# Kernel tuning notes

Hardware: AMD Instinct MI355X
Metric: run time of the kernel (lower is better)

Reference implementation:

```python
import jax, jax.numpy as jnp
import numpy as np

N_HEAD = 16
N_KV = 4
HEAD_DIM = 128
ROPE_BASE = 10000.0
YARN_ORIG = 2048
YARN_TARGET = 8192
YARN_ALPHA = 1.0
YARN_BETA = 1.0
SOFTCAP = 50.0


def _yarn_freqs(seq_len, start=0):
    # inv_freq with YaRN scaling: stretch by (target/orig)**alpha, magnitude 1/beta
    inv_freq = 1.0 / (ROPE_BASE ** (jnp.arange(0, HEAD_DIM, 2, dtype=jnp.float32) / HEAD_DIM))
    scale = (YARN_TARGET / YARN_ORIG) ** YARN_ALPHA
    inv_freq = inv_freq / scale * (1.0 / max(YARN_BETA, 1e-6))
    pos = jnp.arange(start, start + seq_len, dtype=jnp.float32)
    return pos[:, None] * inv_freq[None, :]  # [T, D/2]


def _apply_rope(x, freqs):
    # x: [B, H, T, D], interleaved even/odd rotation
    x_even = x[..., ::2]
    x_odd = x[..., 1::2]
    cos = jnp.cos(freqs)[None, None]  # [1,1,T,D/2]
    sin = jnp.sin(freqs)[None, None]
    y_even = x_even * cos - x_odd * sin
    y_odd = x_odd * cos + x_even * sin
    y = jnp.stack([y_even, y_odd], axis=-1).reshape(x.shape)
    return y


def setup_inputs() -> dict:
    key = jax.random.key(0)
    k1, k2, k3 = jax.random.split(key, 3)
    B, T, C = 2, 2048, 2048
    qkv_dim = (N_HEAD + 2 * N_KV) * HEAD_DIM  # 3072
    x = jax.random.normal(k1, (B, T, C), dtype=jnp.float32)
    w_qkv = jax.random.normal(k2, (C, qkv_dim), dtype=jnp.float32) * (1.0 / np.sqrt(C))
    w_o = jax.random.normal(k3, (C, C), dtype=jnp.float32) * (1.0 / np.sqrt(C))
    return {"x": x, "w_qkv": w_qkv, "w_o": w_o}


def reference(x, w_qkv, w_o):
    B, T, C = x.shape
    qkv = x @ w_qkv  # [B, T, (H+2*Hkv)*D]
    q_dim = N_HEAD * HEAD_DIM
    kv_dim = N_KV * HEAD_DIM
    q = qkv[..., :q_dim].reshape(B, T, N_HEAD, HEAD_DIM).transpose(0, 2, 1, 3)
    k = qkv[..., q_dim:q_dim + kv_dim].reshape(B, T, N_KV, HEAD_DIM).transpose(0, 2, 1, 3)
    v = qkv[..., q_dim + kv_dim:].reshape(B, T, N_KV, HEAD_DIM).transpose(0, 2, 1, 3)

    freqs = _yarn_freqs(T)
    q = _apply_rope(q, freqs)
    k = _apply_rope(k, freqs)

    # GQA: expand kv heads to query heads
    rep = N_HEAD // N_KV
    k = jnp.repeat(k, rep, axis=1)
    v = jnp.repeat(v, rep, axis=1)

    scores = jnp.einsum('bhqd,bhkd->bhqk', q, k) / jnp.sqrt(jnp.float32(HEAD_DIM))
    scores = SOFTCAP * jnp.tanh(scores / SOFTCAP)
    causal = jnp.tril(jnp.ones((T, T), dtype=bool))
    scores = jnp.where(causal[None, None], scores, jnp.float32(-1e9))
    attn = jax.nn.softmax(scores.astype(jnp.float32), axis=-1).astype(q.dtype)
    out = jnp.einsum('bhqk,bhkd->bhqd', attn, v)
    out = out.transpose(0, 2, 1, 3).reshape(B, T, C)
    return out @ w_o
```

## Files before the change

kernel.cpp:

```cpp
#include <hip/hip_runtime.h>
#include <hip/hip_bf16.h>

typedef __attribute__((ext_vector_type(8))) __bf16 bf16x8;
typedef __attribute__((ext_vector_type(2))) __bf16 bf16x2;
typedef __attribute__((ext_vector_type(4))) float f32x4;

#define T_SEQ 2048
#define C_DIM 2048
#define QKV_DIM 3072
#define NKV 4
#define HD 128

#define AS1 __attribute__((address_space(1)))
#define AS3 __attribute__((address_space(3)))

__device__ __forceinline__ unsigned short f2bf(float x) {
    __hip_bfloat16 h = __float2bfloat16(x);
    return __builtin_bit_cast(unsigned short, h);
}
__device__ __forceinline__ float bf2f(unsigned short u) {
    unsigned int i = ((unsigned int)u) << 16;
    return __builtin_bit_cast(float, i);
}
__device__ __forceinline__ unsigned int pkbf(float lo, float hi) {
#if __has_builtin(__builtin_amdgcn_cvt_pk_bf16_f32)
    bf16x2 r = __builtin_amdgcn_cvt_pk_bf16_f32(lo, hi);
    return __builtin_bit_cast(unsigned int, r);
#else
    return ((unsigned int)f2bf(hi) << 16) | (unsigned int)f2bf(lo);
#endif
}
__device__ __forceinline__ f32x4 mfma16(bf16x8 a, bf16x8 b, f32x4 c) {
    return __builtin_amdgcn_mfma_f32_16x16x32_bf16(a, b, c, 0, 0, 0);
}
__device__ __forceinline__ void gload_lds16(const void* g, void* l) {
    __builtin_amdgcn_global_load_lds((const AS1 unsigned int*)g,
                                     (AS3 unsigned int*)l, 16, 0, 0);
}

__global__ __launch_bounds__(256) void cast_f32_to_bf16(
        const float* __restrict__ in, unsigned short* __restrict__ out, int n4) {
    int i = blockIdx.x * 256 + threadIdx.x;
    if (i >= n4) return;
    float4 v = ((const float4*)in)[i];
    uint2 o;
    o.x = pkbf(v.x, v.y);
    o.y = pkbf(v.z, v.w);
    ((uint2*)out)[i] = o;
}

__global__ __launch_bounds__(256) void transpose_cast_f32_bf16(
        const float* __restrict__ in, unsigned short* __restrict__ out,
        int rows, int cols) {
    __shared__ float tile[32][33];
    int c0 = blockIdx.x * 32, r0 = blockIdx.y * 32;
    int tx = threadIdx.x, ty = threadIdx.y;
    #pragma unroll
    for (int i = 0; i < 4; i++)
        tile[ty + 8 * i][tx] = in[(size_t)(r0 + ty + 8 * i) * cols + c0 + tx];
    __syncthreads();
    #pragma unroll
    for (int i = 0; i < 4; i++)
        out[(size_t)(c0 + ty + 8 * i) * rows + r0 + tx] = f2bf(tile[tx][ty + 8 * i]);
}

__global__ __launch_bounds__(256) void pack_k(
        const unsigned short* __restrict__ qkv, unsigned short* __restrict__ kpack) {
    int sid = blockIdx.x;
    int tid = threadIdx.x;
    int row = tid >> 4;
    int chunk = tid & 15;
    int b = sid >> 9, kv = (sid >> 7) & 3, st = sid & 127;
    int t_ = st * 16 + row;
    const unsigned short* src =
        qkv + (size_t)(b * T_SEQ + t_) * QKV_DIM + 2048 + kv * HD + chunk * 8;
    unsigned short* dst = kpack + (size_t)sid * 2048 + chunk * 128 + row * 8;
    *(uint4*)dst = *(const uint4*)src;
}

__global__ __launch_bounds__(256) void pack_v(
        const unsigned short* __restrict__ qkv, unsigned short* __restrict__ vpack) {
    __shared__ unsigned short tile[32][33];
    int c0 = blockIdx.x * 32;
    int r0 = blockIdx.y * 32;
    int tx = threadIdx.x, ty = threadIdx.y;
    #pragma unroll
    for (int i = 0; i < 4; i++)
        tile[ty + 8 * i][tx] =
            qkv[(size_t)(r0 + ty + 8 * i) * QKV_DIM + 2560 + c0 + tx];
    __syncthreads();
    #pragma unroll
    for (int i = 0; i < 4; i++) {
        int dcol = c0 + ty + 8 * i;
        int kv = dcol >> 7, d = dcol & 127;
        int r = r0 + tx;
        int b = r >> 11, t = r & (T_SEQ - 1);
        vpack[(size_t)((b * NKV + kv) * 64 + (t >> 5)) * 4096 +
              (d >> 4) * 512 + ((t >> 3) & 3) * 128 + (d & 15) * 8 + (t & 7)] =
            tile[tx][ty + 8 * i];
    }
}

__global__ __launch_bounds__(256) void yarn_tab_kernel(float2* __restrict__ tab) {
    int idx = blockIdx.x * 256 + threadIdx.x;
    int t = idx >> 6, i = idx & 63;
    float inv = 0.25f * exp2f(-(float)i * (13.287712379549449f / 64.0f));
    float ang = (float)t * inv;
    float s, c;
    __sincosf(ang, &s, &c);
    tab[idx] = make_float2(c, s);
}

__global__ __launch_bounds__(256) void rope_kernel(
        unsigned short* __restrict__ qkv, const float2* __restrict__ tab) {
    int row = blockIdx.x;
    int t = row & (T_SEQ - 1);
    const float2* tb = tab + t * 64;
    for (int p = threadIdx.x; p < 1280; p += 256) {
        int head = p >> 6, i = p & 63;
        float2 cs = tb[i];
        size_t idx = (size_t)row * QKV_DIM + head * 128 + 2 * i;
        unsigned int u = *(const unsigned int*)(qkv + idx);
        float e = bf2f((unsigned short)(u & 0xffff));
        float o = bf2f((unsigned short)(u >> 16));
        *(unsigned int*)(qkv + idx) = pkbf(e * cs.x - o * cs.y, o * cs.x + e * cs.y);
    }
}

template <int OUT_BF16>
__global__ __launch_bounds__(256) void gemm_bt(
        const unsigned short* __restrict__ A, const unsigned short* __restrict__ Bt,
        void* __restrict__ Cout, int M, int N, int K) {
    __shared__ __align__(16) unsigned short As[128 * 32];
    __shared__ __align__(16) unsigned short Bs[128 * 32];
    int tid = threadIdx.x;
    int m0 = blockIdx.y * 128, n0 = blockIdx.x * 128;
    int wave = tid >> 6, lane = tid & 63;
    int wm = (wave & 1) * 64, wn = (wave >> 1) * 64;
    int l15 = lane & 15, quad = lane >> 4;
    int lrow = lane >> 2, lcol = (lane & 3) * 8;

    f32x4 zf = {0.f, 0.f, 0.f, 0.f};
    f32x4 acc[4][4];
    #pragma unroll
    for (int i = 0; i < 4; i++)
        #pragma unroll
        for (int j = 0; j < 4; j++) acc[i][j] = zf;

    int ca = wave * 2;
    const unsigned short* gA = A + (size_t)(m0 + ca * 16 + lrow) * K + lcol;
    const unsigned short* gB = Bt + (size_t)(n0 + ca * 16 + lrow) * K + lcol;

    for (int k0 = 0; k0 < K; k0 += 32) {
        gload_lds16(gA + k0, &As[ca * 512]);
        gload_lds16(gA + k0 + 16 * (size_t)K, &As[ca * 512 + 512]);
        gload_lds16(gB + k0, &Bs[ca * 512]);
        gload_lds16(gB + k0 + 16 * (size_t)K, &Bs[ca * 512 + 512]);
        __syncthreads();
        bf16x8 af[4], bfr[4];
        #pragma unroll
        for (int i = 0; i < 4; i++)
            af[i] = *(const bf16x8*)&As[(wm + i * 16 + l15) * 32 + quad * 8];
        #pragma unroll
        for (int i = 0; i < 4; i++)
            bfr[i] = *(const bf16x8*)&Bs[(wn + i * 16 + l15) * 32 + quad * 8];
        #pragma unroll
        for (int mi = 0; mi < 4; mi++)
            #pragma unroll
            for (int ni = 0; ni < 4; ni++)
                acc[mi][ni] = mfma16(af[mi], bfr[ni], acc[mi][ni]);
        __syncthreads();
    }
    #pragma unroll
    for (int mi = 0; mi < 4; mi++)
        #pragma unroll
        for (int ni = 0; ni < 4; ni++) {
            int row = m0 + wm + mi * 16 + quad * 4;
            int col = n0 + wn + ni * 16 + l15;
            #pragma unroll
            for (int r = 0; r < 4; r++) {
                float v = acc[mi][ni][r];
                if (OUT_BF16)
                    ((unsigned short*)Cout)[(size_t)(row + r) * N + col] = f2bf(v);
                else
                    ((float*)Cout)[(size_t)(row + r) * N + col] = v;
            }
        }
}

__device__ __forceinline__ void attn_pair(
        const unsigned short* __restrict__ qkv,
        const unsigned short* __restrict__ kpack,
        const unsigned short* __restrict__ vpack,
        unsigned short* __restrict__ attn_out,
        unsigned int* __restrict__ pT, float* __restrict__ comb,
        int b, int h, int j, int wave, int lane) {
    int l15 = lane & 15, quad = lane >> 4;
    int kv = h >> 2;
    f32x4 zf = {0.f, 0.f, 0.f, 0.f};

    const float K1 = 0.0051006972f;
    const float K2 = -144.26950408889634f;
    const float K3 = 72.13475204444817f;

    const unsigned short* kb_ = kpack + ((size_t)(b * NKV + kv) * 128) * 2048 + lane * 8;
    const unsigned short* vb_ = vpack + ((size_t)(b * NKV + kv) * 64) * 4096 + lane * 8;

    for (int pass = 0; pass < 2; pass++) {
        int qt = pass ? (127 - j) : j;
        int n = (qt >> 1) + 1;
        int half = n >> 1;
        int lo = wave ? half : 0;
        int hi = wave ? n : half;

        const unsigned short* qp =
            qkv + (size_t)(b * T_SEQ + qt * 16 + l15) * QKV_DIM + h * HD + quad * 8;
        bf16x8 aq[4];
        #pragma unroll
        for (int c = 0; c < 4; c++) aq[c] = *(const bf16x8*)(qp + c * 32);

        f32x4 oacc[8];
        #pragma unroll
        for (int d = 0; d < 8; d++) oacc[d] = zf;
        float lsum = 0.f;
        int qglob = qt * 16 + l15;

        if (lo < hi) {
            bf16x8 KA[8], KB[8];
            auto loadK = [&](bf16x8* K, int t) {
                const unsigned short* a = kb_ + (size_t)t * 4096;
                #pragma unroll
                for (int c = 0; c < 4; c++) {
                    K[c]     = *(const bf16x8*)(a + c * 512);
                    K[4 + c] = *(const bf16x8*)(a + 2048 + c * 512);
                }
            };
            auto step = [&](const bf16x8* K, unsigned int* buf, int t,
                            bf16x8* Kpre, bool do_pre) {
                const unsigned short* v0 = vb_ + (size_t)t * 4096;
                bf16x8 Vv[8];
                #pragma unroll
                for (int dd = 0; dd < 8; dd++)
                    Vv[dd] = *(const bf16x8*)(v0 + dd * 512);
                if (do_pre) loadK(Kpre, t + 1);
                f32x4 s0 = zf, s1 = zf;
                #pragma unroll
                for (int c = 0; c < 4; c++) {
                    s0 = mfma16(K[c], aq[c], s0);
                    s1 = mfma16(K[4 + c], aq[c], s1);
                }
                bool masked = (t == n - 1);
                float p0[4], p1[4];
                int kb = t * 32 + quad * 4;
                #pragma unroll
                for (int r = 0; r < 4; r++) {
                    float e0 = exp2f(s0[r] * K1);
                    float e1 = exp2f(s1[r] * K1);
                    float q0 = exp2f(fmaf(K2, __builtin_amdgcn_rcpf(e0 + 1.f), K3));
                    float q1 = exp2f(fmaf(K2, __builtin_amdgcn_rcpf(e1 + 1.f), K3));
                    if (masked) {
                        q0 = (kb + r <= qglob) ? q0 : 0.f;
                        q1 = (kb + 16 + r <= qglob) ? q1 : 0.f;
                    }
                    p0[r] = q0; p1[r] = q1;
                    lsum += q0 + q1;
                }
                unsigned int d0 = pkbf(p0[0], p0[1]), d1 = pkbf(p0[2], p0[3]);
                unsigned int d2 = pkbf(p1[0], p1[1]), d3 = pkbf(p1[2], p1[3]);
                unsigned int* wp = buf + l15 * 20 + quad * 2;
                *(uint2*)wp = make_uint2(d0, d1);
                *(uint2*)(wp + 8) = make_uint2(d2, d3);
                __asm__ volatile("s_waitcnt lgkmcnt(0)" ::: "memory");
                bf16x8 bp = *(const bf16x8*)(buf + l15 * 20 + quad * 4);
                #pragma unroll
                for (int dd = 0; dd < 8; dd++) oacc[dd] = mfma16(Vv[dd], bp, oacc[dd]);
            };

            loadK(KA, lo);
            int t = lo;
            while (true) {
                bool last = (t == hi - 1);
                step(KA, pT, t, KB, !last);
                if (last) break;
                t++;
                last = (t == hi - 1);
                step(KB, pT + 320, t, KA, !last);
                if (last) break;
                t++;
            }
        }

        float* cl = comb + lane * 34;
        if (wave == 0) {
            #pragma unroll
            for (int dd = 0; dd < 8; dd++)
                #pragma unroll
                for (int r = 0; r < 4; r++) cl[dd * 4 + r] = oacc[dd][r];
            cl[32] = lsum;
        }
        __syncthreads();
        if (wave == 1) {
            #pragma unroll
            for (int dd = 0; dd < 8; dd++)
                #pragma unroll
                for (int r = 0; r < 4; r++) oacc[dd][r] += cl[dd * 4 + r];
            lsum += cl[32];
            float l = lsum;
            l += __shfl_xor(l, 16);
            l += __shfl_xor(l, 32);
            float rl = __builtin_amdgcn_rcpf(l);
            unsigned short* op = attn_out +
                (size_t)(b * T_SEQ + qt * 16 + l15) * C_DIM + h * HD + quad * 4;
            #pragma unroll
            for (int dd = 0; dd < 8; dd++) {
                unsigned int u0 = pkbf(oacc[dd][0] * rl, oacc[dd][1] * rl);
                unsigned int u1 = pkbf(oacc[dd][2] * rl, oacc[dd][3] * rl);
                *(uint2*)(op + dd * 16) = make_uint2(u0, u1);
            }
        }
        __syncthreads();
    }
}

__global__ __launch_bounds__(128, 2) void attn_kernel(
        const unsigned short* __restrict__ qkv,
        const unsigned short* __restrict__ kpack,
        const unsigned short* __restrict__ vpack,
        unsigned short* __restrict__ attn_out) {
    __shared__ __align__(16) unsigned int pT[2][640];
    __shared__ float comb[64 * 34];
    int bid = blockIdx.x;
    int g = bid & 7, i = bid >> 3;
    int b = g >> 2, kv = g & 3;
    int hh = (i >> 6) & 3, j = i & 63;
    int h = kv * 4 + hh;
    int wave = threadIdx.x >> 6, lane = threadIdx.x & 63;
    attn_pair(qkv, kpack, vpack, attn_out, pT[wave], comb, b, h, j, wave, lane);
}

extern "C" void kernel_launch(void* const* d_in, const int* in_sizes, int n_in,
                              void* d_out, int out_size, void* d_ws, size_t ws_size,
                              hipStream_t stream) {
    (void)in_sizes; (void)n_in; (void)out_size; (void)ws_size;
    const float* x = (const float*)d_in[0];
    const float* w_qkv = (const float*)d_in[1];
    const float* w_o = (const float*)d_in[2];
    char* ws = (char*)d_ws;

    unsigned short* xbf   = (unsigned short*)(ws);
    unsigned short* wqkvT = (unsigned short*)(ws + 16777216);
    unsigned short* woT   = (unsigned short*)(ws + 29360128);
    unsigned short* qkv   = (unsigned short*)(ws + 37748736);
    unsigned short* kpack = (unsigned short*)(ws + 16777216);
    unsigned short* vpack = (unsigned short*)(ws + 20971520);
    float2*         tab   = (float2*)(ws + 62914560);
    unsigned short* attn  = xbf;

    cast_f32_to_bf16<<<8192, 256, 0, stream>>>(x, xbf, 2097152);
    transpose_cast_f32_bf16<<<dim3(96, 64), dim3(32, 8), 0, stream>>>(w_qkv, wqkvT, 2048, 3072);
    transpose_cast_f32_bf16<<<dim3(64, 64), dim3(32, 8), 0, stream>>>(w_o, woT, 2048, 2048);
    yarn_tab_kernel<<<512, 256, 0, stream>>>(tab);
    gemm_bt<1><<<dim3(24, 32), 256, 0, stream>>>(xbf, wqkvT, qkv, 4096, 3072, 2048);
    rope_kernel<<<4096, 256, 0, stream>>>(qkv, tab);
    pack_k<<<1024, 256, 0, stream>>>(qkv, kpack);
    pack_v<<<dim3(16, 128), dim3(32, 8), 0, stream>>>(qkv, vpack);
    attn_kernel<<<2048, 128, 0, stream>>>(qkv, kpack, vpack, attn);
    gemm_bt<0><<<dim3(16, 32), 256, 0, stream>>>(attn, woT, d_out, 4096, 2048, 2048);
}
```

Before: 350.6 us.

## Process two GQA query heads per attention block to reuse K/V loads

Each attention block now handles two query heads that share a KV head, so every K and V tile loaded from global memory feeds twice as many MFMAs. The grid is halved and the shared P buffers and combine buffers are doubled. The final cross-wave reduction is split so each wave finalises one head. Register pressure roughly doubles for the accumulators, and the launch_bounds occupancy hint was dropped, which may lower occupancy or cause spills.

```diff
diff --git a/kernel.cpp b/kernel.cpp
--- a/kernel.cpp
+++ b/kernel.cpp
@@ -194,9 +194,9 @@
         const unsigned short* __restrict__ vpack,
         unsigned short* __restrict__ attn_out,
         unsigned int* __restrict__ pT, float* __restrict__ comb,
-        int b, int h, int j, int wave, int lane) {
+        int b, int hA, int j, int wave, int lane) {
     int l15 = lane & 15, quad = lane >> 4;
-    int kv = h >> 2;
+    int kv = hA >> 2;
     f32x4 zf = {0.f, 0.f, 0.f, 0.f};
 
     const float K1 = 0.0051006972f;
@@ -205,6 +205,9 @@
 
     const unsigned short* kb_ = kpack + ((size_t)(b * NKV + kv) * 128) * 2048 + lane * 8;
     const unsigned short* vb_ = vpack + ((size_t)(b * NKV + kv) * 64) * 4096 + lane * 8;
+
+    float* myStore = comb + (wave * 64 + lane) * 34;
+    float* peer    = comb + ((1 - wave) * 64 + lane) * 34;
 
     for (int pass = 0; pass < 2; pass++) {
         int qt = pass ? (127 - j) : j;
@@ -214,15 +217,18 @@
         int hi = wave ? n : half;
 
         const unsigned short* qp =
-            qkv + (size_t)(b * T_SEQ + qt * 16 + l15) * QKV_DIM + h * HD + quad * 8;
-        bf16x8 aq[4];
-        #pragma unroll
-        for (int c = 0; c < 4; c++) aq[c] = *(const bf16x8*)(qp + c * 32);
-
-        f32x4 oacc[8];
-        #pragma unroll
-        for (int d = 0; d < 8; d++) oacc[d] = zf;
-        float lsum = 0.f;
+            qkv + (size_t)(b * T_SEQ + qt * 16 + l15) * QKV_DIM + hA * HD + quad * 8;
+        bf16x8 aqA[4], aqB[4];
+        #pragma unroll
+        for (int c = 0; c < 4; c++) {
+            aqA[c] = *(const bf16x8*)(qp + c * 32);
+            aqB[c] = *(const bf16x8*)(qp + HD + c * 32);
+        }
+
+        f32x4 oA[8], oB[8];
+        #pragma unroll
+        for (int d = 0; d < 8; d++) { oA[d] = zf; oB[d] = zf; }
+        float lsA = 0.f, lsB = 0.f;
         int qglob = qt * 16 + l15;
 
         if (lo < hi) {
@@ -243,37 +249,47 @@
                 for (int dd = 0; dd < 8; dd++)
                     Vv[dd] = *(const bf16x8*)(v0 + dd * 512);
                 if (do_pre) loadK(Kpre, t + 1);
-                f32x4 s0 = zf, s1 = zf;
+                f32x4 s0A = zf, s1A = zf, s0B = zf, s1B = zf;
                 #pragma unroll
                 for (int c = 0; c < 4; c++) {
-                    s0 = mfma16(K[c], aq[c], s0);
-                    s1 = mfma16(K[4 + c], aq[c], s1);
+                    s0A = mfma16(K[c],     aqA[c], s0A);
+                    s1A = mfma16(K[4 + c], aqA[c], s1A);
+                    s0B = mfma16(K[c],     aqB[c], s0B);
+                    s1B = mfma16(K[4 + c], aqB[c], s1B);
                 }
                 bool masked = (t == n - 1);
-                float p0[4], p1[4];
+                float p0A[4], p1A[4], p0B[4], p1B[4];
                 int kb = t * 32 + quad * 4;
                 #pragma unroll
                 for (int r = 0; r < 4; r++) {
-                    float e0 = exp2f(s0[r] * K1);
-                    float e1 = exp2f(s1[r] * K1);
-                    float q0 = exp2f(fmaf(K2, __builtin_amdgcn_rcpf(e0 + 1.f), K3));
-                    float q1 = exp2f(fmaf(K2, __builtin_amdgcn_rcpf(e1 + 1.f), K3));
+                    float e0A = exp2f(s0A[r] * K1), e1A = exp2f(s1A[r] * K1);
+                    float e0B = exp2f(s0B[r] * K1), e1B = exp2f(s1B[r] * K1);
+                    float q0A = exp2f(fmaf(K2, __builtin_amdgcn_rcpf(e0A + 1.f), K3));
+                    float q1A = exp2f(fmaf(K2, __builtin_amdgcn_rcpf(e1A + 1.f), K3));
+                    float q0B = exp2f(fmaf(K2, __builtin_amdgcn_rcpf(e0B + 1.f), K3));
+                    float q1B = exp2f(fmaf(K2, __builtin_amdgcn_rcpf(e1B + 1.f), K3));
                     if (masked) {
-                        q0 = (kb + r <= qglob) ? q0 : 0.f;
-                        q1 = (kb + 16 + r <= qglob) ? q1 : 0.f;
+                        bool m0 = (kb + r <= qglob), m1 = (kb + 16 + r <= qglob);
+                        q0A = m0 ? q0A : 0.f;  q1A = m1 ? q1A : 0.f;
+                        q0B = m0 ? q0B : 0.f;  q1B = m1 ? q1B : 0.f;
                     }
-                    p0[r] = q0; p1[r] = q1;
-                    lsum += q0 + q1;
+                    p0A[r] = q0A; p1A[r] = q1A; lsA += q0A + q1A;
+                    p0B[r] = q0B; p1B[r] = q1B; lsB += q0B + q1B;
                 }
-                unsigned int d0 = pkbf(p0[0], p0[1]), d1 = pkbf(p0[2], p0[3]);
-                unsigned int d2 = pkbf(p1[0], p1[1]), d3 = pkbf(p1[2], p1[3]);
-                unsigned int* wp = buf + l15 * 20 + quad * 2;
-                *(uint2*)wp = make_uint2(d0, d1);
-                *(uint2*)(wp + 8) = make_uint2(d2, d3);
+                unsigned int* wpA = buf + l15 * 20 + quad * 2;
+                unsigned int* wpB = wpA + 320;
+                *(uint2*)wpA       = make_uint2(pkbf(p0A[0], p0A[1]), pkbf(p0A[2], p0A[3]));
+                *(uint2*)(wpA + 8) = make_uint2(pkbf(p1A[0], p1A[1]), pkbf(p1A[2], p1A[3]));
+                *(uint2*)wpB       = make_uint2(pkbf(p0B[0], p0B[1]), pkbf(p0B[2], p0B[3]));
+                *(uint2*)(wpB + 8) = make_uint2(pkbf(p1B[0], p1B[1]), pkbf(p1B[2], p1B[3]));
                 __asm__ volatile("s_waitcnt lgkmcnt(0)" ::: "memory");
-                bf16x8 bp = *(const bf16x8*)(buf + l15 * 20 + quad * 4);
-                #pragma unroll
-                for (int dd = 0; dd < 8; dd++) oacc[dd] = mfma16(Vv[dd], bp, oacc[dd]);
+                bf16x8 bpA = *(const bf16x8*)(buf + l15 * 20 + quad * 4);
+                bf16x8 bpB = *(const bf16x8*)(buf + 320 + l15 * 20 + quad * 4);
+                #pragma unroll
+                for (int dd = 0; dd < 8; dd++) {
+                    oA[dd] = mfma16(Vv[dd], bpA, oA[dd]);
+                    oB[dd] = mfma16(Vv[dd], bpB, oB[dd]);
+                }
             };
 
             loadK(KA, lo);
@@ -284,37 +300,41 @@
                 if (last) break;
                 t++;
                 last = (t == hi - 1);
-                step(KB, pT + 320, t, KA, !last);
+                step(KB, pT + 640, t, KA, !last);
                 if (last) break;
                 t++;
             }
         }
 
-        float* cl = comb + lane * 34;
-        if (wave == 0) {
+        {
+            f32x4* po = wave ? oA : oB;
+            float pls = wave ? lsA : lsB;
             #pragma unroll
             for (int dd = 0; dd < 8; dd++)
                 #pragma unroll
-                for (int r = 0; r < 4; r++) cl[dd * 4 + r] = oacc[dd][r];
-            cl[32] = lsum;
+                for (int r = 0; r < 4; r++) myStore[dd * 4 + r] = po[dd][r];
+            myStore[32] = pls;
         }
         __syncthreads();
-        if (wave == 1) {
+        {
+            f32x4* mo = wave ? oB : oA;
+            float mls = wave ? lsB : lsA;
             #pragma unroll
             for (int dd = 0; dd < 8; dd++)
                 #pragma unroll
-                for (int r = 0; r < 4; r++) oacc[dd][r] += cl[dd * 4 + r];
-            lsum += cl[32];
-            float l = lsum;
+                for (int r = 0; r < 4; r++) mo[dd][r] += peer[dd * 4 + r];
+            mls += peer[32];
+            float l = mls;
             l += __shfl_xor(l, 16);
             l += __shfl_xor(l, 32);
             float rl = __builtin_amdgcn_rcpf(l);
+            int h = hA + wave;
             unsigned short* op = attn_out +
                 (size_t)(b * T_SEQ + qt * 16 + l15) * C_DIM + h * HD + quad * 4;
             #pragma unroll
             for (int dd = 0; dd < 8; dd++) {
-                unsigned int u0 = pkbf(oacc[dd][0] * rl, oacc[dd][1] * rl);
-                unsigned int u1 = pkbf(oacc[dd][2] * rl, oacc[dd][3] * rl);
+                unsigned int u0 = pkbf(mo[dd][0] * rl, mo[dd][1] * rl);
+                unsigned int u1 = pkbf(mo[dd][2] * rl, mo[dd][3] * rl);
                 *(uint2*)(op + dd * 16) = make_uint2(u0, u1);
             }
         }
@@ -322,20 +342,20 @@
     }
 }
 
-__global__ __launch_bounds__(128, 2) void attn_kernel(
+__global__ __launch_bounds__(128) void attn_kernel(
         const unsigned short* __restrict__ qkv,
         const unsigned short* __restrict__ kpack,
         const unsigned short* __restrict__ vpack,
         unsigned short* __restrict__ attn_out) {
-    __shared__ __align__(16) unsigned int pT[2][640];
-    __shared__ float comb[64 * 34];
+    __shared__ __align__(16) unsigned int pT[2][1280];
+    __shared__ float comb[2 * 64 * 34];
     int bid = blockIdx.x;
     int g = bid & 7, i = bid >> 3;
     int b = g >> 2, kv = g & 3;
-    int hh = (i >> 6) & 3, j = i & 63;
-    int h = kv * 4 + hh;
+    int hp = (i >> 6) & 1, j = i & 63;
+    int hA = kv * 4 + hp * 2;
     int wave = threadIdx.x >> 6, lane = threadIdx.x & 63;
-    attn_pair(qkv, kpack, vpack, attn_out, pT[wave], comb, b, h, j, wave, lane);
+    attn_pair(qkv, kpack, vpack, attn_out, pT[wave], comb, b, hA, j, wave, lane);
 }
 
 extern "C" void kernel_launch(void* const* d_in, const int* in_sizes, int n_in,
@@ -364,6 +384,6 @@
     rope_kernel<<<4096, 256, 0, stream>>>(qkv, tab);
     pack_k<<<1024, 256, 0, stream>>>(qkv, kpack);
     pack_v<<<dim3(16, 128), dim3(32, 8), 0, stream>>>(qkv, vpack);
-    attn_kernel<<<2048, 128, 0, stream>>>(qkv, kpack, vpack, attn);
+    attn_kernel<<<1024, 128, 0, stream>>>(qkv, kpack, vpack, attn);
     gemm_bt<0><<<dim3(16, 32), 256, 0, stream>>>(attn, woT, d_out, 4096, 2048, 2048);
 }
```

New measurement: 347.9 us. Within noise of the previous version (-0.8%).
